# Kernel tuning notes

Hardware: AMD Instinct MI355X
Metric: run time of the kernel (lower is better)

The kernel has to match this reference:

```python
import jax, jax.numpy as jnp
import numpy as np

STRIDE = 4
RADIUS = 2
ALPHA = 0.5
SMOOTH = 1e-06

# Precompute static disk-offset stencil (pixels with dy^2+dx^2 <= r^2).
_dy, _dx = np.meshgrid(np.arange(-RADIUS, RADIUS + 1), np.arange(-RADIUS, RADIUS + 1), indexing='ij')
_keep = (_dy ** 2 + _dx ** 2) <= RADIUS * RADIUS
DY = jnp.asarray(_dy[_keep], dtype=jnp.int32)  # [K]
DX = jnp.asarray(_dx[_keep], dtype=jnp.int32)  # [K]


def _points_to_masks(points, H, W):
    """Vectorized disk rasterization. points: [B,N,2] int (x,y) in original coords.
    Returns gt masks [B,1,H,W] float32."""
    cx = points[..., 0] // STRIDE  # [B,N]
    cy = points[..., 1] // STRIDE  # [B,N]
    center_ok = (cx >= 0) & (cx < W) & (cy >= 0) & (cy < H)
    yy = cy[..., None] + DY  # [B,N,K]
    xx = cx[..., None] + DX  # [B,N,K]
    valid = center_ok[..., None] & (yy >= 0) & (yy < H) & (xx >= 0) & (xx < W)
    B = points.shape[0]
    b = jnp.arange(B, dtype=jnp.int32)[:, None, None]
    flat = b * (H * W) + yy * W + xx
    flat = jnp.where(valid, flat, 0)
    vals = valid.astype(jnp.float32)
    m = jnp.zeros((B * H * W,), jnp.float32).at[flat.ravel()].max(vals.ravel())
    return m.reshape(B, 1, H, W)


def setup_inputs() -> dict:
    key = jax.random.key(0)
    k1, k2 = jax.random.split(key)
    B, H, W, N = 16, 1024, 1024, 2000
    pred_logits = jax.random.normal(k1, (B, 1, H, W), dtype=jnp.float32)
    points = jax.random.randint(k2, (B, N, 2), 0, H * STRIDE, dtype=jnp.int32)
    return {"pred_logits": pred_logits, "points": points}


def reference(pred_logits, points):
    B, _, H, W = pred_logits.shape
    gt = _points_to_masks(points, H, W)  # [B,1,H,W]
    # pos_weight computed from the gt mask (detached scalar in the original)
    pos = gt.sum()
    neg = gt.size - pos
    pos_weight = neg / (pos + SMOOTH)
    # BCE-with-logits: -[pw*y*log(sig(x)) + (1-y)*log(1-sig(x))]
    bce = jnp.mean(pos_weight * gt * jax.nn.softplus(-pred_logits)
                   + (1.0 - gt) * jax.nn.softplus(pred_logits))
    prob = jax.nn.sigmoid(pred_logits)
    intersection = (prob * gt).sum(axis=(1, 2, 3))
    union = prob.sum(axis=(1, 2, 3)) + gt.sum(axis=(1, 2, 3))
    dice = 1.0 - jnp.mean((2.0 * intersection + SMOOTH) / (union + SMOOTH))
    return ALPHA * bce + (1.0 - ALPHA) * dice
```

## Files before the change

### kernel.cpp

```cpp
#include <hip/hip_runtime.h>

constexpr int B = 16, H = 1024, W = 1024, N = 2000;
constexpr int HW = H * W;
constexpr long long TOT = (long long)B * HW;
constexpr float SMOOTH = 1e-6f;

typedef float f32x4 __attribute__((ext_vector_type(4)));

constexpr size_t MASK_WORDS = (size_t)B * HW / 32;
constexpr size_t MASK_BYTES = MASK_WORDS * 4;

constexpr int BLOCKS_PER_BATCH = 128;
constexpr int NBLOCKS = B * BLOCKS_PER_BATCH;
constexpr int THREADS = 256;
constexpr int UNROLL = 8;

__global__ void raster_kernel(const int* __restrict__ pts,
                              unsigned int* __restrict__ mask) {
    int t = blockIdx.x * blockDim.x + threadIdx.x;
    if (t >= B * N) return;
    int b = t / N;
    int x = pts[2 * t + 0];
    int y = pts[2 * t + 1];
    int cx = x >> 2;
    int cy = y >> 2;
    if (cx < 0 || cx >= W || cy < 0 || cy >= H) return;
    const int dy[13] = {-2, -1, -1, -1,  0, 0, 0, 0, 0,  1, 1, 1,  2};
    const int dx[13] = { 0, -1,  0,  1, -2,-1, 0, 1, 2, -1, 0, 1,  0};
    unsigned int base = (unsigned int)b * HW;
#pragma unroll
    for (int k = 0; k < 13; ++k) {
        int yy = cy + dy[k];
        int xx = cx + dx[k];
        if (yy >= 0 && yy < H && xx >= 0 && xx < W) {
            unsigned int idx = base + (unsigned int)yy * W + (unsigned int)xx;
            atomicOr(&mask[idx >> 5], 1u << (idx & 31));
        }
    }
}

__device__ inline float wave_reduce(float v) {
#pragma unroll
    for (int o = 32; o > 0; o >>= 1) v += __shfl_down(v, o, 64);
    return v;
}

__global__ __launch_bounds__(THREADS)
void mainpass_kernel(const float* __restrict__ logits,
                     const unsigned int* __restrict__ mask,
                     float* __restrict__ part) {
    const int blk = blockIdx.x;
    const int b = blk / BLOCKS_PER_BATCH;
    const int chunk = blk % BLOCKS_PER_BATCH;
    const int base_v = b * (HW / 4) + chunk * (UNROLL * THREADS);
    const int tid = threadIdx.x;

    const f32x4* __restrict__ vlog = reinterpret_cast<const f32x4*>(logits);

    f32x4 xv[UNROLL];
    unsigned int mw[UNROLL];
#pragma unroll
    for (int it = 0; it < UNROLL; ++it) {
        int v = base_v + it * THREADS + tid;
        xv[it] = vlog[v];
        mw[it] = mask[(unsigned int)v >> 3];
    }

    float sA = 0.f, sBg = 0.f, sCg = 0.f, si = 0.f, spr = 0.f, sg = 0.f;

#pragma unroll
    for (int it = 0; it < UNROLL; ++it) {
        int v = base_v + it * THREADS + tid;
        unsigned int bits = mw[it] >> ((v & 7) * 4);
#pragma unroll
        for (int j = 0; j < 4; ++j) {
            float x = xv[it][j];
            float g = (float)((bits >> j) & 1u);
            float ax = fabsf(x);
            float t = __builtin_amdgcn_exp2f(-1.44269504f * ax);
            float u = 1.0f + t;
            float l = __builtin_amdgcn_logf(u) * 0.69314718f;
            float sp = l + fmaxf(x, 0.f);
            float r = __builtin_amdgcn_rcpf(u);
            float prob = r * ((x >= 0.f) ? 1.0f : t);
            sA += sp;
            sBg += g * sp;
            sCg += g * x;
            si += g * prob;
            spr += prob;
            sg += g;
        }
    }

    __shared__ float red[4][6];
    int lane = threadIdx.x & 63;
    int wv = threadIdx.x >> 6;
    sA = wave_reduce(sA);
    sBg = wave_reduce(sBg);
    sCg = wave_reduce(sCg);
    si = wave_reduce(si);
    spr = wave_reduce(spr);
    sg = wave_reduce(sg);
    if (lane == 0) {
        red[wv][0] = sA; red[wv][1] = sBg; red[wv][2] = sCg;
        red[wv][3] = si; red[wv][4] = spr; red[wv][5] = sg;
    }
    __syncthreads();
    if (threadIdx.x == 0) {
        float a[6] = {0, 0, 0, 0, 0, 0};
#pragma unroll
        for (int w = 0; w < 4; ++w)
#pragma unroll
            for (int q = 0; q < 6; ++q) a[q] += red[w][q];
#pragma unroll
        for (int q = 0; q < 6; ++q) part[q * NBLOCKS + blk] = a[q];
    }
}

__global__ __launch_bounds__(256)
void reduce_finalize_kernel(const float* __restrict__ part,
                            float* __restrict__ out) {
    const int tid = threadIdx.x;
    const int lane = tid & 63;
    const int wv = tid >> 6;

    float a0 = 0.f, a1 = 0.f, a2 = 0.f;
#pragma unroll
    for (int k = 0; k < NBLOCKS / 256; ++k) {
        int i = tid + 256 * k;
        a0 += part[0 * NBLOCKS + i];
        a1 += part[1 * NBLOCKS + i];
        a2 += part[2 * NBLOCKS + i];
    }
    a0 = wave_reduce(a0);
    a1 = wave_reduce(a1);
    a2 = wave_reduce(a2);
    __shared__ float redg[4][3];
    if (lane == 0) { redg[wv][0] = a0; redg[wv][1] = a1; redg[wv][2] = a2; }

    int b = tid >> 4;
    int j = tid & 15;
    float p3 = 0.f, p4 = 0.f, p5 = 0.f;
#pragma unroll
    for (int k = 0; k < BLOCKS_PER_BATCH / 16; ++k) {
        int idx = b * BLOCKS_PER_BATCH + j + 16 * k;
        p3 += part[3 * NBLOCKS + idx];
        p4 += part[4 * NBLOCKS + idx];
        p5 += part[5 * NBLOCKS + idx];
    }
#pragma unroll
    for (int m = 1; m < 16; m <<= 1) {
        p3 += __shfl_xor(p3, m, 64);
        p4 += __shfl_xor(p4, m, 64);
        p5 += __shfl_xor(p5, m, 64);
    }
    __shared__ float sI[16], sP[16], sG[16];
    if (j == 0) { sI[b] = p3; sP[b] = p4; sG[b] = p5; }
    __syncthreads();

    if (tid == 0) {
        float A = 0.f, Bg = 0.f, Cg = 0.f;
#pragma unroll
        for (int w = 0; w < 4; ++w) {
            A += redg[w][0]; Bg += redg[w][1]; Cg += redg[w][2];
        }
        float S1 = Bg - Cg;
        float S2 = A - Bg;
        float pos = 0.f;
#pragma unroll
        for (int bb = 0; bb < B; ++bb) pos += sG[bb];
        float neg = (float)TOT - pos;
        float pw = neg / (pos + SMOOTH);
        float bce = (pw * S1 + S2) / (float)TOT;
        float dsum = 0.f;
#pragma unroll
        for (int bb = 0; bb < B; ++bb) {
            dsum += (2.f * sI[bb] + SMOOTH) / (sP[bb] + sG[bb] + SMOOTH);
        }
        float dice = 1.f - dsum / (float)B;
        out[0] = 0.5f * bce + 0.5f * dice;
    }
}

extern "C" void kernel_launch(void* const* d_in, const int* in_sizes, int n_in,
                              void* d_out, int out_size, void* d_ws, size_t ws_size,
                              hipStream_t stream) {
    const float* logits = (const float*)d_in[0];
    const int* pts = (const int*)d_in[1];
    unsigned int* mask = (unsigned int*)d_ws;
    float* part = (float*)((char*)d_ws + MASK_BYTES);

    (void)hipMemsetAsync(d_ws, 0, MASK_BYTES, stream);

    raster_kernel<<<(B * N + 255) / 256, 256, 0, stream>>>(pts, mask);

    mainpass_kernel<<<NBLOCKS, THREADS, 0, stream>>>(logits, mask, part);

    reduce_finalize_kernel<<<1, 256, 0, stream>>>(part, (float*)d_out);
}
```

Baseline: 48.10 us.

## Fuse final reduction into main pass via last-block counter; replace memset with kernel

Drops the separate single-block finalize kernel. Each main-pass block publishes its partials, bumps an atomic counter, and whichever block arrives last does the global reduction and writes the loss. The hipMemsetAsync of the mask is replaced by a small vectorized zero kernel that also resets the counter. This removes one kernel launch and the memset dispatch, at the cost of an atomic per block and a serialized tail reduction inside the last block.

```diff
diff --git a/kernel.cpp b/kernel.cpp
--- a/kernel.cpp
+++ b/kernel.cpp
@@ -6,6 +6,7 @@
 constexpr float SMOOTH = 1e-6f;
 
 typedef float f32x4 __attribute__((ext_vector_type(4)));
+typedef unsigned int u32x4 __attribute__((ext_vector_type(4)));
 
 constexpr size_t MASK_WORDS = (size_t)B * HW / 32;
 constexpr size_t MASK_BYTES = MASK_WORDS * 4;
@@ -14,9 +15,18 @@
 constexpr int NBLOCKS = B * BLOCKS_PER_BATCH;
 constexpr int THREADS = 256;
 constexpr int UNROLL = 8;
-
-__global__ void raster_kernel(const int* __restrict__ pts,
-                              unsigned int* __restrict__ mask) {
+constexpr int PART_FLOATS = 6 * NBLOCKS;
+
+__global__ __launch_bounds__(256)
+void zero_kernel(u32x4* __restrict__ maskv, unsigned int* __restrict__ ctr) {
+    int t = blockIdx.x * 256 + threadIdx.x;
+    maskv[t] = (u32x4)(0u);
+    if (t == 0) *ctr = 0u;
+}
+
+__global__ __launch_bounds__(256)
+void raster_kernel(const int* __restrict__ pts,
+                   unsigned int* __restrict__ mask) {
     int t = blockIdx.x * blockDim.x + threadIdx.x;
     if (t >= B * N) return;
     int b = t / N;
@@ -48,7 +58,9 @@
 __global__ __launch_bounds__(THREADS)
 void mainpass_kernel(const float* __restrict__ logits,
                      const unsigned int* __restrict__ mask,
-                     float* __restrict__ part) {
+                     float* __restrict__ part,
+                     unsigned int* __restrict__ ctr,
+                     float* __restrict__ out) {
     const int blk = blockIdx.x;
     const int b = blk / BLOCKS_PER_BATCH;
     const int chunk = blk % BLOCKS_PER_BATCH;
@@ -93,8 +105,8 @@
     }
 
     __shared__ float red[4][6];
-    int lane = threadIdx.x & 63;
-    int wv = threadIdx.x >> 6;
+    const int lane = tid & 63;
+    const int wv = tid >> 6;
     sA = wave_reduce(sA);
     sBg = wave_reduce(sBg);
     sCg = wave_reduce(sCg);
@@ -106,31 +118,36 @@
         red[wv][3] = si; red[wv][4] = spr; red[wv][5] = sg;
     }
     __syncthreads();
-    if (threadIdx.x == 0) {
+
+    __shared__ int slast;
+    if (tid == 0) {
         float a[6] = {0, 0, 0, 0, 0, 0};
 #pragma unroll
         for (int w = 0; w < 4; ++w)
 #pragma unroll
             for (int q = 0; q < 6; ++q) a[q] += red[w][q];
 #pragma unroll
-        for (int q = 0; q < 6; ++q) part[q * NBLOCKS + blk] = a[q];
-    }
-}
-
-__global__ __launch_bounds__(256)
-void reduce_finalize_kernel(const float* __restrict__ part,
-                            float* __restrict__ out) {
-    const int tid = threadIdx.x;
-    const int lane = tid & 63;
-    const int wv = tid >> 6;
+        for (int q = 0; q < 6; ++q)
+            __hip_atomic_store(&part[q * NBLOCKS + blk], a[q],
+                               __ATOMIC_RELAXED, __HIP_MEMORY_SCOPE_AGENT);
+        unsigned int old = __hip_atomic_fetch_add(ctr, 1u, __ATOMIC_ACQ_REL,
+                                                  __HIP_MEMORY_SCOPE_AGENT);
+        slast = (old == (unsigned int)(NBLOCKS - 1)) ? 1 : 0;
+    }
+    __syncthreads();
+    if (!slast) return;
+
 
     float a0 = 0.f, a1 = 0.f, a2 = 0.f;
 #pragma unroll
     for (int k = 0; k < NBLOCKS / 256; ++k) {
         int i = tid + 256 * k;
-        a0 += part[0 * NBLOCKS + i];
-        a1 += part[1 * NBLOCKS + i];
-        a2 += part[2 * NBLOCKS + i];
+        a0 += __hip_atomic_load(&part[0 * NBLOCKS + i], __ATOMIC_RELAXED,
+                                __HIP_MEMORY_SCOPE_AGENT);
+        a1 += __hip_atomic_load(&part[1 * NBLOCKS + i], __ATOMIC_RELAXED,
+                                __HIP_MEMORY_SCOPE_AGENT);
+        a2 += __hip_atomic_load(&part[2 * NBLOCKS + i], __ATOMIC_RELAXED,
+                                __HIP_MEMORY_SCOPE_AGENT);
     }
     a0 = wave_reduce(a0);
     a1 = wave_reduce(a1);
@@ -138,15 +155,18 @@
     __shared__ float redg[4][3];
     if (lane == 0) { redg[wv][0] = a0; redg[wv][1] = a1; redg[wv][2] = a2; }
 
-    int b = tid >> 4;
+    int bb = tid >> 4;
     int j = tid & 15;
     float p3 = 0.f, p4 = 0.f, p5 = 0.f;
 #pragma unroll
     for (int k = 0; k < BLOCKS_PER_BATCH / 16; ++k) {
-        int idx = b * BLOCKS_PER_BATCH + j + 16 * k;
-        p3 += part[3 * NBLOCKS + idx];
-        p4 += part[4 * NBLOCKS + idx];
-        p5 += part[5 * NBLOCKS + idx];
+        int idx = bb * BLOCKS_PER_BATCH + j + 16 * k;
+        p3 += __hip_atomic_load(&part[3 * NBLOCKS + idx], __ATOMIC_RELAXED,
+                                __HIP_MEMORY_SCOPE_AGENT);
+        p4 += __hip_atomic_load(&part[4 * NBLOCKS + idx], __ATOMIC_RELAXED,
+                                __HIP_MEMORY_SCOPE_AGENT);
+        p5 += __hip_atomic_load(&part[5 * NBLOCKS + idx], __ATOMIC_RELAXED,
+                                __HIP_MEMORY_SCOPE_AGENT);
     }
 #pragma unroll
     for (int m = 1; m < 16; m <<= 1) {
@@ -155,7 +175,7 @@
         p5 += __shfl_xor(p5, m, 64);
     }
     __shared__ float sI[16], sP[16], sG[16];
-    if (j == 0) { sI[b] = p3; sP[b] = p4; sG[b] = p5; }
+    if (j == 0) { sI[bb] = p3; sP[bb] = p4; sG[bb] = p5; }
     __syncthreads();
 
     if (tid == 0) {
@@ -168,14 +188,14 @@
         float S2 = A - Bg;
         float pos = 0.f;
 #pragma unroll
-        for (int bb = 0; bb < B; ++bb) pos += sG[bb];
+        for (int k = 0; k < B; ++k) pos += sG[k];
         float neg = (float)TOT - pos;
         float pw = neg / (pos + SMOOTH);
         float bce = (pw * S1 + S2) / (float)TOT;
         float dsum = 0.f;
 #pragma unroll
-        for (int bb = 0; bb < B; ++bb) {
-            dsum += (2.f * sI[bb] + SMOOTH) / (sP[bb] + sG[bb] + SMOOTH);
+        for (int k = 0; k < B; ++k) {
+            dsum += (2.f * sI[k] + SMOOTH) / (sP[k] + sG[k] + SMOOTH);
         }
         float dice = 1.f - dsum / (float)B;
         out[0] = 0.5f * bce + 0.5f * dice;
@@ -189,12 +209,14 @@
     const int* pts = (const int*)d_in[1];
     unsigned int* mask = (unsigned int*)d_ws;
     float* part = (float*)((char*)d_ws + MASK_BYTES);
-
-    (void)hipMemsetAsync(d_ws, 0, MASK_BYTES, stream);
+    unsigned int* ctr = (unsigned int*)((char*)d_ws + MASK_BYTES +
+                                        (size_t)PART_FLOATS * 4);
+
+    zero_kernel<<<(int)(MASK_WORDS / 4 / 256), 256, 0, stream>>>(
+        reinterpret_cast<u32x4*>(mask), ctr);
 
     raster_kernel<<<(B * N + 255) / 256, 256, 0, stream>>>(pts, mask);
 
-    mainpass_kernel<<<NBLOCKS, THREADS, 0, stream>>>(logits, mask, part);
-
-    reduce_finalize_kernel<<<1, 256, 0, stream>>>(part, (float*)d_out);
-}
+    mainpass_kernel<<<NBLOCKS, THREADS, 0, stream>>>(logits, mask, part, ctr,
+                                                     (float*)d_out);
+}
```

Measured after the change: 99.26 us. 106% more time.
